# Kernel tuning notes

Hardware: AMD Instinct MI355X
Metric: run time of the kernel (lower is better)

Reference implementation:

```python
import jax, jax.numpy as jnp
import numpy as np


def conv1x1(x, w, b):
    # x: (B,C,H,W), w: (O,C), b: (O,) -- 1x1 conv == channel matmul
    return jnp.einsum('bchw,oc->bohw', x, w) + b[None, :, None, None]


def setup_inputs() -> dict:
    key = jax.random.key(0)
    B, C, H, W = 4, 256, 64, 64
    Ch = C // 2
    ks = jax.random.split(key, 12)
    s = 0.05
    return {
        'x':    jax.random.normal(ks[0], (B, C, H, W), jnp.float32),
        'wf1':  jax.random.normal(ks[1], (Ch, C), jnp.float32) * s,
        'bf1':  jnp.zeros((Ch,), jnp.float32),
        'wf2':  jax.random.normal(ks[2], (Ch, Ch), jnp.float32) * s,
        'bf2':  jnp.zeros((Ch,), jnp.float32),
        'wg1':  jax.random.normal(ks[3], (Ch, C), jnp.float32) * s,
        'bg1':  jnp.zeros((Ch,), jnp.float32),
        'wg2':  jax.random.normal(ks[4], (Ch, Ch), jnp.float32) * s,
        'bg2':  jnp.zeros((Ch,), jnp.float32),
        'wh':   jax.random.normal(ks[5], (C, C), jnp.float32) * s,
        'bh':   jnp.zeros((C,), jnp.float32),
        'gamma': jnp.full((1,), 0.5, jnp.float32),
    }


def reference(x, wf1, bf1, wf2, bf2, wg1, bg1, wg2, bg2, wh, bh, gamma):
    B, C, H, W = x.shape
    N = H * W
    # f_ and g_: conv1x1 -> relu -> conv1x1, projecting C -> C/2
    f = conv1x1(jax.nn.relu(conv1x1(x, wf1, bf1)), wf2, bf2).reshape(B, -1, N)  # (B,C/2,N)
    g = conv1x1(jax.nn.relu(conv1x1(x, wg1, bg1)), wg2, bg2).reshape(B, -1, N)  # (B,C/2,N)
    h = conv1x1(x, wh, bh).reshape(B, C, N)                                     # (B,C,N)
    # attn_dist = bmm(f^T, g): (B, N, N)
    attn = jnp.einsum('bcn,bcm->bnm', f, g)
    # softmax over dim=1 (the query axis) -- non-standard axis, as in source
    attn_soft = jax.nn.softmax(attn, axis=1)
    out = jnp.einsum('bcn,bnm->bcm', h, attn_soft).reshape(B, C, H, W)
    out = gamma[0] * out + x  # skip connection
    return out, attn_soft.reshape(B, H, W, N)
```

## Files before the change

### kernel.cpp

```cpp
#include <hip/hip_runtime.h>

typedef unsigned short u16;
typedef unsigned int   u32;
typedef float  floatx4 __attribute__((ext_vector_type(4)));
typedef __bf16 bfx8    __attribute__((ext_vector_type(8)));
typedef u16    u16x8   __attribute__((ext_vector_type(8)));

#define DEV __device__ __forceinline__

#define NB 4
#define NC 256
#define NCH 128
#define NSP 4096
#define OUT_OFF 4194304

DEV u16 f2bf(float f) {
  u32 u = __builtin_bit_cast(u32, f);
  u = (u + 0x7fffu + ((u >> 16) & 1u)) >> 16;
  return (u16)u;
}

DEV float bf2f(u16 h) {
  u32 w = (u32)h << 16;
  return __builtin_bit_cast(float, w);
}

DEV void lds_load16(const u16* g, u16* l) {
  __builtin_amdgcn_global_load_lds(
      (const __attribute__((address_space(1))) u32*)g,
      (__attribute__((address_space(3))) u32*)l, 16, 0, 0);
}

DEV floatx4 mfma16(bfx8 a, bfx8 b, floatx4 c) {
  return __builtin_amdgcn_mfma_f32_16x16x32_bf16(a, b, c, 0, 0, 0);
}

DEV float rsum16(float v) {
  #pragma unroll
  for (int m = 1; m < 16; m <<= 1) v += __shfl_xor(v, m, 64);
  return v;
}

__global__ __launch_bounds__(256) void cvt_all(
    const float* __restrict__ wf1, const float* __restrict__ wg1,
    const float* __restrict__ wf2, const float* __restrict__ wg2,
    const float* __restrict__ wh,
    u16* __restrict__ wfg1b, u16* __restrict__ wfg2b, u16* __restrict__ whb,
    float* __restrict__ rs,
    const float* __restrict__ bf1, const float* __restrict__ bg1,
    const float* __restrict__ bf2, const float* __restrict__ bg2,
    float* __restrict__ bfg1, float* __restrict__ bfg2) {
  int i = blockIdx.x * 256 + threadIdx.x;
  if (i < 32768) { wfg1b[i] = f2bf(wf1[i]); return; }
  i -= 32768;
  if (i < 32768) { wfg1b[32768 + i] = f2bf(wg1[i]); return; }
  i -= 32768;
  if (i < 16384) { wfg2b[i] = f2bf(wf2[i]); return; }
  i -= 16384;
  if (i < 16384) { wfg2b[16384 + i] = f2bf(wg2[i]); return; }
  i -= 16384;
  if (i < 65536) { whb[i] = f2bf(wh[i]); return; }
  i -= 65536;
  if (i < NB * NSP) { rs[i] = 0.f; return; }
  i -= NB * NSP;
  if (i < 128) { bfg1[i] = bf1[i]; return; }
  i -= 128;
  if (i < 128) { bfg1[128 + i] = bg1[i]; return; }
  i -= 128;
  if (i < 128) { bfg2[i] = bf2[i]; return; }
  i -= 128;
  if (i < 128) { bfg2[128 + i] = bg2[i]; return; }
}

__global__ __launch_bounds__(256) void transpose_x(const float* __restrict__ x,
                                                   u16* __restrict__ xT) {
  __shared__ float T[64 * 65];
  const int b = blockIdx.z, c0 = blockIdx.y * 64, n0 = blockIdx.x * 64;
  const int tid = threadIdx.x;
  const int j = tid & 63, r0 = tid >> 6;
  const size_t xbase = ((size_t)b * NC + c0) * NSP + n0;
  #pragma unroll
  for (int s = 0; s < 16; s++) {
    int cl = s * 4 + r0;
    T[cl * 65 + j] = x[xbase + (size_t)cl * NSP + j];
  }
  __syncthreads();
  const size_t tbase = ((size_t)b * NSP + n0) * NC + c0;
  #pragma unroll
  for (int s = 0; s < 16; s++) {
    int nr = s * 4 + r0;
    xT[tbase + (size_t)nr * NC + j] = f2bf(T[j * 65 + nr]);
  }
}

template<int BM, int BN, int BK, int BIAS, bool RELU, bool OUTBF16, bool FINAL,
         bool SWZ>
__global__ __launch_bounds__(256) void gemm_bt_k(
    const u16* __restrict__ A, long long sA, int lda,
    const u16* __restrict__ Bt, long long sB, int ldb,
    void* __restrict__ C, long long sC, int ldc,
    int K, const float* __restrict__ bias, int sbias,
    const float* __restrict__ gamma, const float* __restrict__ xres,
    const float* __restrict__ rsv) {
  constexpr int TM = BM / 32, TN = BN / 32, KS = BK / 32;
  constexpr int ASZ = BM * BK, BSZ = BN * BK;
  __shared__ u16 As[2][ASZ];
  __shared__ u16 Bs[2][BSZ];
  int bx = blockIdx.x, by = blockIdx.y, bz = blockIdx.z;
  if constexpr (SWZ) {
    const int gx = gridDim.x, gy = gridDim.y;
    const int nwg = gx * gy * gridDim.z;
    const int bid = (bz * gy + by) * gx + bx;
    const int lx = (bid & 7) * (nwg >> 3) + (bid >> 3);
    bx = lx % gx;
    const int t = lx / gx;
    by = t % gy;
    bz = t / gy;
  }
  const int b = bz;
  const u16* Ab = A + (size_t)sA * b;
  const u16* Bb = Bt + (size_t)sB * b;
  const int m0 = bx * BM, n0 = by * BN;
  const int tid = threadIdx.x, lane = tid & 63, wave = tid >> 6;
  const int q = lane >> 4, cc = lane & 15;
  const int wm = (wave >> 1) * (BM / 2), wn = (wave & 1) * (BN / 2);

  auto stage = [&](int p, int k0) {
    #pragma unroll
    for (int i = 0; i < ASZ / 2048; i++) {
      int slot = i * 256 + tid;
      int fr = slot / (64 * KS);
      int ks = (slot / 64) % KS;
      int qq = (slot >> 4) & 3, cq = slot & 15;
      lds_load16(Ab + (size_t)(m0 + fr * 16 + cq) * lda + k0 + ks * 32 + qq * 8,
                 &As[p][slot * 8]);
    }
    #pragma unroll
    for (int i = 0; i < BSZ / 2048; i++) {
      int slot = i * 256 + tid;
      int fr = slot / (64 * KS);
      int ks = (slot / 64) % KS;
      int qq = (slot >> 4) & 3, cq = slot & 15;
      lds_load16(Bb + (size_t)(n0 + fr * 16 + cq) * ldb + k0 + ks * 32 + qq * 8,
                 &Bs[p][slot * 8]);
    }
  };

  floatx4 acc[TM][TN];
  #pragma unroll
  for (int mi = 0; mi < TM; mi++)
    #pragma unroll
    for (int ni = 0; ni < TN; ni++)
      acc[mi][ni] = floatx4{0.f, 0.f, 0.f, 0.f};

  stage(0, 0);
  __syncthreads();
  int p = 0;
  for (int k0 = 0; k0 < K; k0 += BK) {
    if (k0 + BK < K) stage(p ^ 1, k0 + BK);
    #pragma unroll
    for (int ks = 0; ks < KS; ks++) {
      bfx8 af[TM], bfr[TN];
      #pragma unroll
      for (int mi = 0; mi < TM; mi++)
        af[mi] = *(const bfx8*)(&As[p][((((wm >> 4) + mi) * KS + ks) * 64 + lane) * 8]);
      #pragma unroll
      for (int ni = 0; ni < TN; ni++)
        bfr[ni] = *(const bfx8*)(&Bs[p][((((wn >> 4) + ni) * KS + ks) * 64 + lane) * 8]);
      #pragma unroll
      for (int mi = 0; mi < TM; mi++)
        #pragma unroll
        for (int ni = 0; ni < TN; ni++)
          acc[mi][ni] = mfma16(af[mi], bfr[ni], acc[mi][ni]);
    }
    __syncthreads();
    p ^= 1;
  }

  float g0 = 0.f;
  if constexpr (FINAL) g0 = gamma[0];
  #pragma unroll
  for (int mi = 0; mi < TM; mi++) {
    #pragma unroll
    for (int ni = 0; ni < TN; ni++) {
      const int col = n0 + wn + ni * 16 + cc;
      float scl = 0.f;
      if constexpr (FINAL) scl = g0 / rsv[(size_t)b * NSP + col];
      #pragma unroll
      for (int r = 0; r < 4; r++) {
        int row = m0 + wm + mi * 16 + q * 4 + r;
        float v = acc[mi][ni][r];
        if constexpr (BIAS == 1) v += bias[b * sbias + col];
        if constexpr (BIAS == 2) v += bias[b * sbias + row];
        if constexpr (RELU) v = fmaxf(v, 0.f);
        size_t idx = (size_t)sC * b + (size_t)row * ldc + col;
        if constexpr (FINAL) v = v * scl + xres[idx];
        if constexpr (OUTBF16) ((u16*)C)[idx] = f2bf(v);
        else ((float*)C)[idx] = v;
      }
    }
  }
}

__global__ __launch_bounds__(256) void attn_se_k(
    const u16* __restrict__ gT, const u16* __restrict__ fT,
    float* __restrict__ rsum, u16* __restrict__ pT) {
  __shared__ u16 Bs[64 * 128];
  __shared__ u16 Pb[64 * 72];
  const int b = blockIdx.z, m0 = blockIdx.y * 64, n0 = blockIdx.x * 512;
  const int tid = threadIdx.x, lane = tid & 63, wave = tid >> 6;
  const int q = lane >> 4, cc = lane & 15;
  const size_t bN = (size_t)b * NSP;

  bfx8 af[4];
  {
    const u16* gA = gT + (bN + m0 + wave * 16 + cc) * NCH;
    #pragma unroll
    for (int ks = 0; ks < 4; ks++) af[ks] = *(const bfx8*)(gA + ks * 32 + q * 8);
  }
  float ps[4] = {0.f, 0.f, 0.f, 0.f};

  for (int sc = 0; sc < 8; sc++) {
    const int nc = n0 + sc * 64;
    #pragma unroll
    for (int i = 0; i < 4; i++) {
      int slot = i * 256 + tid;
      int ni = slot >> 8, ks = (slot >> 6) & 3;
      int qq = (slot >> 4) & 3, cq = slot & 15;
      lds_load16(fT + (bN + nc + ni * 16 + cq) * NCH + ks * 32 + qq * 8,
                 Bs + slot * 8);
    }
    __syncthreads();
    #pragma unroll
    for (int ni = 0; ni < 4; ni++) {
      floatx4 s = floatx4{0.f, 0.f, 0.f, 0.f};
      #pragma unroll
      for (int ks = 0; ks < 4; ks++) {
        bfx8 bfr = *(const bfx8*)(Bs + ((ni * 4 + ks) * 64 + lane) * 8);
        s = mfma16(af[ks], bfr, s);
      }
      #pragma unroll
      for (int r = 0; r < 4; r++) {
        float e = __expf(fminf(s[r], 80.f));
        ps[r] += e;
        Pb[(wave * 16 + q * 4 + r) * 72 + ni * 16 + cc] = f2bf(e);
      }
    }
    __syncthreads();
    #pragma unroll
    for (int i = 0; i < 2; i++) {
      int slot = i * 256 + tid;
      int ml = slot >> 3, c8 = slot & 7;
      u16x8 v = *(const u16x8*)(Pb + ml * 72 + c8 * 8);
      *(u16x8*)(pT + (bN + m0 + ml) * NSP + nc + c8 * 8) = v;
    }
  }
  #pragma unroll
  for (int r = 0; r < 4; r++) ps[r] = rsum16(ps[r]);
  if (cc == 0) {
    #pragma unroll
    for (int r = 0; r < 4; r++)
      atomicAdd(&rsum[bN + m0 + wave * 16 + q * 4 + r], ps[r]);
  }
}

__global__ __launch_bounds__(256) void attn_norm_k(
    const u16* __restrict__ pT, const float* __restrict__ rs,
    float* __restrict__ outP) {
  __shared__ u16 T[64 * 257];
  __shared__ float rinvs[256];
  const int b = blockIdx.z, n0 = blockIdx.x * 64, m0 = blockIdx.y * 256;
  const int tid = threadIdx.x;
  const size_t bN = (size_t)b * NSP;

  rinvs[tid] = 1.f / rs[bN + m0 + tid];
  #pragma unroll
  for (int i = 0; i < 8; i++) {
    int slot = i * 256 + tid;
    int mi = slot >> 3, c8 = slot & 7;
    u16x8 v = *(const u16x8*)(pT + (bN + m0 + mi) * NSP + n0 + c8 * 8);
    #pragma unroll
    for (int j = 0; j < 8; j++) T[(c8 * 8 + j) * 257 + mi] = v[j];
  }
  __syncthreads();
  #pragma unroll
  for (int i = 0; i < 16; i++) {
    int slot = i * 256 + tid;
    int nl = slot >> 6, f4 = slot & 63;
    floatx4 rv = *(const floatx4*)(rinvs + f4 * 4);
    const u16* tr = T + nl * 257 + f4 * 4;
    floatx4 o;
    #pragma unroll
    for (int k = 0; k < 4; k++) o[k] = bf2f(tr[k]) * rv[k];
    *(floatx4*)(outP + (bN + n0 + nl) * NSP + m0 + f4 * 4) = o;
  }
}

extern "C" void kernel_launch(void* const* d_in, const int* in_sizes, int n_in,
                              void* d_out, int out_size, void* d_ws, size_t ws_size,
                              hipStream_t stream) {
  const float* x     = (const float*)d_in[0];
  const float* wf1   = (const float*)d_in[1];
  const float* bf1   = (const float*)d_in[2];
  const float* wf2   = (const float*)d_in[3];
  const float* bf2   = (const float*)d_in[4];
  const float* wg1   = (const float*)d_in[5];
  const float* bg1   = (const float*)d_in[6];
  const float* wg2   = (const float*)d_in[7];
  const float* bg2   = (const float*)d_in[8];
  const float* wh    = (const float*)d_in[9];
  const float* bh    = (const float*)d_in[10];
  const float* gamma = (const float*)d_in[11];
  float* out = (float*)d_out;

  char* ws = (char*)d_ws;
  size_t off = 0;
  auto alloc = [&](size_t bytes) -> char* {
    char* p = ws + off;
    off += (bytes + 255) & ~(size_t)255;
    return p;
  };
  u16* wfg1b = (u16*)alloc((size_t)256 * 256 * 2);
  u16* wfg2b = (u16*)alloc((size_t)2 * 128 * 128 * 2);
  u16* whb   = (u16*)alloc((size_t)NC * NC * 2);
  float* bfg1 = (float*)alloc(256 * 4);
  float* bfg2 = (float*)alloc(256 * 4);
  u16* xT   = (u16*)alloc((size_t)NB * NSP * NC * 2);
  u16* fg1T = (u16*)alloc((size_t)NB * NSP * 256 * 2);
  u16* fTb  = (u16*)alloc((size_t)NB * NSP * NCH * 2);
  u16* gTb  = (u16*)alloc((size_t)NB * NSP * NCH * 2);
  u16* hb   = (u16*)alloc((size_t)NB * NC * NSP * 2);
  float* rs = (float*)alloc((size_t)NB * NSP * 4);
  u16* pTb  = (u16*)alloc((size_t)NB * NSP * NSP * 2);

  cvt_all<<<dim3(707), 256, 0, stream>>>(wf1, wg1, wf2, wg2, wh,
                                         wfg1b, wfg2b, whb,
                                         rs, bf1, bg1, bf2, bg2, bfg1, bfg2);
  transpose_x<<<dim3(NSP / 64, NC / 64, NB), 256, 0, stream>>>(x, xT);

  const long long sX = (long long)NSP * NC;
  const long long sH = (long long)NC * NSP;
  const long long sP = (long long)NSP * NSP;
  const long long sFG = (long long)NB * NSP * NCH;

  gemm_bt_k<64, 128, 64, 1, true, true, false, false>
      <<<dim3(256, 2, 1), 256, 0, stream>>>(
      xT, 0, NC, wfg1b, 0, NC, fg1T, 0, 256, NC, bfg1, 0,
      nullptr, nullptr, nullptr);
  gemm_bt_k<64, 128, 64, 1, false, true, false, false>
      <<<dim3(256, 1, 2), 256, 0, stream>>>(
      fg1T, 128, 256, wfg2b, 128 * 128, NCH, fTb, sFG, NCH, NCH, bfg2, 128,
      nullptr, nullptr, nullptr);
  gemm_bt_k<64, 128, 64, 2, false, true, false, false>
      <<<dim3(4, 32, NB), 256, 0, stream>>>(
      whb, 0, NC, xT, sX, NC, hb, sH, NSP, NC, bh, 0,
      nullptr, nullptr, nullptr);

  attn_se_k<<<dim3(8, 64, NB), 256, 0, stream>>>(gTb, fTb, rs, pTb);

  gemm_bt_k<128, 64, 64, 0, false, false, true, true>
      <<<dim3(2, 64, NB), 256, 0, stream>>>(
      hb, sH, NSP, pTb, sP, NSP, out, sH, NSP, NSP, nullptr, 0,
      gamma, x, rs);

  attn_norm_k<<<dim3(NSP / 64, NSP / 256, NB), 256, 0, stream>>>(
      pTb, rs, out + OUT_OFF);

  (void)in_sizes; (void)n_in; (void)out_size; (void)ws_size;
}
```

Measured before the change: 494.9 us.

## Fuse score/exp kernel with output GEMM into single attention kernel

Replaces the separate exp-score kernel (with atomic row sums) and the final h·P GEMM with one kernel. For each 64-column query block it computes the scores over all key tiles, exponentiates them, and immediately multiplies them by h tiles staged in LDS. The softmax denominators are accumulated locally, which removes the atomics and the zeroing pass. This avoids re-reading the full bf16 P matrix in the output GEMM, but P is still written for the normalized attention output. In exchange, each block now serializes 64 tiles with two barriers per tile and has only 256 blocks of 512 threads, so occupancy may be lower.

```diff
diff --git a/kernel.cpp b/kernel.cpp
--- a/kernel.cpp
+++ b/kernel.cpp
@@ -5,6 +5,7 @@
 typedef float  floatx4 __attribute__((ext_vector_type(4)));
 typedef __bf16 bfx8    __attribute__((ext_vector_type(8)));
 typedef u16    u16x8   __attribute__((ext_vector_type(8)));
+typedef u32    u32x4   __attribute__((ext_vector_type(4)));
 
 #define DEV __device__ __forceinline__
 
@@ -35,18 +36,11 @@
   return __builtin_amdgcn_mfma_f32_16x16x32_bf16(a, b, c, 0, 0, 0);
 }
 
-DEV float rsum16(float v) {
-  #pragma unroll
-  for (int m = 1; m < 16; m <<= 1) v += __shfl_xor(v, m, 64);
-  return v;
-}
-
 __global__ __launch_bounds__(256) void cvt_all(
     const float* __restrict__ wf1, const float* __restrict__ wg1,
     const float* __restrict__ wf2, const float* __restrict__ wg2,
     const float* __restrict__ wh,
     u16* __restrict__ wfg1b, u16* __restrict__ wfg2b, u16* __restrict__ whb,
-    float* __restrict__ rs,
     const float* __restrict__ bf1, const float* __restrict__ bg1,
     const float* __restrict__ bf2, const float* __restrict__ bg2,
     float* __restrict__ bfg1, float* __restrict__ bfg2) {
@@ -61,8 +55,6 @@
   i -= 16384;
   if (i < 65536) { whb[i] = f2bf(wh[i]); return; }
   i -= 65536;
-  if (i < NB * NSP) { rs[i] = 0.f; return; }
-  i -= NB * NSP;
   if (i < 128) { bfg1[i] = bf1[i]; return; }
   i -= 128;
   if (i < 128) { bfg1[128 + i] = bg1[i]; return; }
@@ -93,34 +85,20 @@
   }
 }
 
-template<int BM, int BN, int BK, int BIAS, bool RELU, bool OUTBF16, bool FINAL,
-         bool SWZ>
+template<int BM, int BN, int BK, int BIAS, bool RELU, bool OUTBF16>
 __global__ __launch_bounds__(256) void gemm_bt_k(
     const u16* __restrict__ A, long long sA, int lda,
     const u16* __restrict__ Bt, long long sB, int ldb,
     void* __restrict__ C, long long sC, int ldc,
-    int K, const float* __restrict__ bias, int sbias,
-    const float* __restrict__ gamma, const float* __restrict__ xres,
-    const float* __restrict__ rsv) {
+    int K, const float* __restrict__ bias, int sbias) {
   constexpr int TM = BM / 32, TN = BN / 32, KS = BK / 32;
   constexpr int ASZ = BM * BK, BSZ = BN * BK;
   __shared__ u16 As[2][ASZ];
   __shared__ u16 Bs[2][BSZ];
-  int bx = blockIdx.x, by = blockIdx.y, bz = blockIdx.z;
-  if constexpr (SWZ) {
-    const int gx = gridDim.x, gy = gridDim.y;
-    const int nwg = gx * gy * gridDim.z;
-    const int bid = (bz * gy + by) * gx + bx;
-    const int lx = (bid & 7) * (nwg >> 3) + (bid >> 3);
-    bx = lx % gx;
-    const int t = lx / gx;
-    by = t % gy;
-    bz = t / gy;
-  }
-  const int b = bz;
+  const int b = blockIdx.z;
   const u16* Ab = A + (size_t)sA * b;
   const u16* Bb = Bt + (size_t)sB * b;
-  const int m0 = bx * BM, n0 = by * BN;
+  const int m0 = blockIdx.x * BM, n0 = blockIdx.y * BN;
   const int tid = threadIdx.x, lane = tid & 63, wave = tid >> 6;
   const int q = lane >> 4, cc = lane & 15;
   const int wm = (wave >> 1) * (BM / 2), wn = (wave & 1) * (BN / 2);
@@ -177,15 +155,11 @@
     p ^= 1;
   }
 
-  float g0 = 0.f;
-  if constexpr (FINAL) g0 = gamma[0];
   #pragma unroll
   for (int mi = 0; mi < TM; mi++) {
     #pragma unroll
     for (int ni = 0; ni < TN; ni++) {
       const int col = n0 + wn + ni * 16 + cc;
-      float scl = 0.f;
-      if constexpr (FINAL) scl = g0 / rsv[(size_t)b * NSP + col];
       #pragma unroll
       for (int r = 0; r < 4; r++) {
         int row = m0 + wm + mi * 16 + q * 4 + r;
@@ -194,7 +168,6 @@
         if constexpr (BIAS == 2) v += bias[b * sbias + row];
         if constexpr (RELU) v = fmaxf(v, 0.f);
         size_t idx = (size_t)sC * b + (size_t)row * ldc + col;
-        if constexpr (FINAL) v = v * scl + xres[idx];
         if constexpr (OUTBF16) ((u16*)C)[idx] = f2bf(v);
         else ((float*)C)[idx] = v;
       }
@@ -202,65 +175,143 @@
   }
 }
 
-__global__ __launch_bounds__(256) void attn_se_k(
+__global__ __launch_bounds__(512) void attn_out_k(
     const u16* __restrict__ gT, const u16* __restrict__ fT,
-    float* __restrict__ rsum, u16* __restrict__ pT) {
-  __shared__ u16 Bs[64 * 128];
-  __shared__ u16 Pb[64 * 72];
-  const int b = blockIdx.z, m0 = blockIdx.y * 64, n0 = blockIdx.x * 512;
-  const int tid = threadIdx.x, lane = tid & 63, wave = tid >> 6;
+    const u16* __restrict__ hb, float* __restrict__ rs,
+    u16* __restrict__ pT, float* __restrict__ out,
+    const float* __restrict__ gamma, const float* __restrict__ x) {
+  __shared__ u16 fTl[2][64 * 128];
+  __shared__ u16 hl[256 * 64];
+  __shared__ u32 EL[2048];
+  __shared__ float rsp[8][16];
+  __shared__ float rsinv[64];
+  const int b = blockIdx.z, m0 = blockIdx.x * 64;
+  const int tid = threadIdx.x, lane = tid & 63, w = tid >> 6;
   const int q = lane >> 4, cc = lane & 15;
+  const int khalf = w >> 2, m16w = w & 3;
   const size_t bN = (size_t)b * NSP;
 
-  bfx8 af[4];
+  bfx8 gB[4];
   {
-    const u16* gA = gT + (bN + m0 + wave * 16 + cc) * NCH;
-    #pragma unroll
-    for (int ks = 0; ks < 4; ks++) af[ks] = *(const bfx8*)(gA + ks * 32 + q * 8);
-  }
-  float ps[4] = {0.f, 0.f, 0.f, 0.f};
-
-  for (int sc = 0; sc < 8; sc++) {
-    const int nc = n0 + sc * 64;
+    const u16* gA = gT + (bN + m0 + m16w * 16 + cc) * NCH;
+    #pragma unroll
+    for (int ks = 0; ks < 4; ks++) gB[ks] = *(const bfx8*)(gA + ks * 32 + q * 8);
+  }
+
+  floatx4 oacc[2][4];
+  #pragma unroll
+  for (int cg = 0; cg < 2; cg++)
+    #pragma unroll
+    for (int m16 = 0; m16 < 4; m16++)
+      oacc[cg][m16] = floatx4{0.f, 0.f, 0.f, 0.f};
+  float ps = 0.f;
+
+  auto stage_f = [&](int buf, int nt) {
+    #pragma unroll
+    for (int i = 0; i < 2; i++) {
+      int slot = i * 512 + tid;
+      int fr = slot >> 8, ks = (slot >> 6) & 3;
+      int qq = (slot >> 4) & 3, cq = slot & 15;
+      lds_load16(fT + (bN + nt + fr * 16 + cq) * NCH + ks * 32 + qq * 8,
+                 &fTl[buf][slot * 8]);
+    }
+  };
+  auto stage_h = [&](int nt) {
     #pragma unroll
     for (int i = 0; i < 4; i++) {
-      int slot = i * 256 + tid;
-      int ni = slot >> 8, ks = (slot >> 6) & 3;
+      int slot = i * 512 + tid;
+      int fr = slot >> 7, ks = (slot >> 6) & 1;
       int qq = (slot >> 4) & 3, cq = slot & 15;
-      lds_load16(fT + (bN + nc + ni * 16 + cq) * NCH + ks * 32 + qq * 8,
-                 Bs + slot * 8);
+      lds_load16(hb + ((size_t)b * NC + fr * 16 + cq) * NSP + nt + ks * 32 + qq * 8,
+                 &hl[slot * 8]);
+    }
+  };
+
+  stage_f(0, 0);
+  __syncthreads();
+
+  #pragma unroll 1
+  for (int t = 0; t < 64; t++) {
+    const int nt = t * 64;
+    if (t + 1 < 64) stage_f((t + 1) & 1, nt + 64);
+    stage_h(nt);
+
+    floatx4 sacc[2];
+    sacc[0] = floatx4{0.f, 0.f, 0.f, 0.f};
+    sacc[1] = floatx4{0.f, 0.f, 0.f, 0.f};
+    #pragma unroll
+    for (int ks = 0; ks < 4; ks++) {
+      #pragma unroll
+      for (int ni = 0; ni < 2; ni++) {
+        bfx8 a = *(const bfx8*)(&fTl[t & 1][(((khalf * 2 + ni) * 4 + ks) * 64 + lane) * 8]);
+        sacc[ni] = mfma16(a, gB[ks], sacc[ni]);
+      }
+    }
+    #pragma unroll
+    for (int ni = 0; ni < 2; ni++) {
+      float e[4];
+      #pragma unroll
+      for (int r = 0; r < 4; r++) {
+        e[r] = __expf(fminf(sacc[ni][r], 80.f));
+        ps += e[r];
+      }
+      #pragma unroll
+      for (int r2 = 0; r2 < 2; r2++) {
+        u32 pk = (u32)f2bf(e[2 * r2]) | ((u32)f2bf(e[2 * r2 + 1]) << 16);
+        EL[((m16w * 2 + khalf) * 64 + (2 * ni + (q >> 1)) * 16 + cc) * 4 +
+           2 * (q & 1) + r2] = pk;
+      }
     }
     __syncthreads();
-    #pragma unroll
-    for (int ni = 0; ni < 4; ni++) {
-      floatx4 s = floatx4{0.f, 0.f, 0.f, 0.f};
-      #pragma unroll
-      for (int ks = 0; ks < 4; ks++) {
-        bfx8 bfr = *(const bfx8*)(Bs + ((ni * 4 + ks) * 64 + lane) * 8);
-        s = mfma16(af[ks], bfr, s);
-      }
+
+    #pragma unroll
+    for (int ks = 0; ks < 2; ks++) {
+      bfx8 bf[4];
+      #pragma unroll
+      for (int m16 = 0; m16 < 4; m16++)
+        bf[m16] = *(const bfx8*)((const u16*)&EL[((m16 * 2 + ks) * 64 + lane) * 4]);
+      #pragma unroll
+      for (int cg = 0; cg < 2; cg++) {
+        bfx8 a = *(const bfx8*)(&hl[(((w * 2 + cg) * 2 + ks) * 64 + lane) * 8]);
+        #pragma unroll
+        for (int m16 = 0; m16 < 4; m16++)
+          oacc[cg][m16] = mfma16(a, bf[m16], oacc[cg][m16]);
+      }
+    }
+    {
+      const int fr = tid >> 7, ks2 = (tid >> 6) & 1;
+      const int qv = (tid >> 4) & 3, cv = tid & 15;
+      u32x4 d = *(const u32x4*)(&EL[tid * 4]);
+      *(u32x4*)(pT + (bN + m0 + fr * 16 + cv) * NSP + nt + ks2 * 32 + qv * 8) = d;
+    }
+    __syncthreads();
+  }
+
+  ps += __shfl_xor(ps, 16, 64);
+  ps += __shfl_xor(ps, 32, 64);
+  if (lane < 16) rsp[w][lane] = ps;
+  __syncthreads();
+  if (tid < 64) {
+    float s = rsp[tid >> 4][tid & 15] + rsp[4 + (tid >> 4)][tid & 15];
+    rs[bN + m0 + tid] = s;
+    rsinv[tid] = 1.f / s;
+  }
+  __syncthreads();
+
+  const float g0 = gamma[0];
+  #pragma unroll
+  for (int cg = 0; cg < 2; cg++) {
+    #pragma unroll
+    for (int m16 = 0; m16 < 4; m16++) {
+      const float ri = rsinv[m16 * 16 + cc];
       #pragma unroll
       for (int r = 0; r < 4; r++) {
-        float e = __expf(fminf(s[r], 80.f));
-        ps[r] += e;
-        Pb[(wave * 16 + q * 4 + r) * 72 + ni * 16 + cc] = f2bf(e);
-      }
-    }
-    __syncthreads();
-    #pragma unroll
-    for (int i = 0; i < 2; i++) {
-      int slot = i * 256 + tid;
-      int ml = slot >> 3, c8 = slot & 7;
-      u16x8 v = *(const u16x8*)(Pb + ml * 72 + c8 * 8);
-      *(u16x8*)(pT + (bN + m0 + ml) * NSP + nc + c8 * 8) = v;
-    }
-  }
-  #pragma unroll
-  for (int r = 0; r < 4; r++) ps[r] = rsum16(ps[r]);
-  if (cc == 0) {
-    #pragma unroll
-    for (int r = 0; r < 4; r++)
-      atomicAdd(&rsum[bN + m0 + wave * 16 + q * 4 + r], ps[r]);
+        int c = w * 32 + cg * 16 + q * 4 + r;
+        int m = m16 * 16 + cc;
+        size_t idx = ((size_t)b * NC + c) * NSP + m0 + m;
+        out[idx] = g0 * oacc[cg][m16][r] * ri + x[idx];
+      }
+    }
   }
 }
 
@@ -333,35 +384,24 @@
   float* rs = (float*)alloc((size_t)NB * NSP * 4);
   u16* pTb  = (u16*)alloc((size_t)NB * NSP * NSP * 2);
 
-  cvt_all<<<dim3(707), 256, 0, stream>>>(wf1, wg1, wf2, wg2, wh,
+  cvt_all<<<dim3(641), 256, 0, stream>>>(wf1, wg1, wf2, wg2, wh,
                                          wfg1b, wfg2b, whb,
-                                         rs, bf1, bg1, bf2, bg2, bfg1, bfg2);
+                                         bf1, bg1, bf2, bg2, bfg1, bfg2);
   transpose_x<<<dim3(NSP / 64, NC / 64, NB), 256, 0, stream>>>(x, xT);
 
   const long long sX = (long long)NSP * NC;
   const long long sH = (long long)NC * NSP;
-  const long long sP = (long long)NSP * NSP;
   const long long sFG = (long long)NB * NSP * NCH;
 
-  gemm_bt_k<64, 128, 64, 1, true, true, false, false>
-      <<<dim3(256, 2, 1), 256, 0, stream>>>(
-      xT, 0, NC, wfg1b, 0, NC, fg1T, 0, 256, NC, bfg1, 0,
-      nullptr, nullptr, nullptr);
-  gemm_bt_k<64, 128, 64, 1, false, true, false, false>
-      <<<dim3(256, 1, 2), 256, 0, stream>>>(
-      fg1T, 128, 256, wfg2b, 128 * 128, NCH, fTb, sFG, NCH, NCH, bfg2, 128,
-      nullptr, nullptr, nullptr);
-  gemm_bt_k<64, 128, 64, 2, false, true, false, false>
-      <<<dim3(4, 32, NB), 256, 0, stream>>>(
-      whb, 0, NC, xT, sX, NC, hb, sH, NSP, NC, bh, 0,
-      nullptr, nullptr, nullptr);
-
-  attn_se_k<<<dim3(8, 64, NB), 256, 0, stream>>>(gTb, fTb, rs, pTb);
-
-  gemm_bt_k<128, 64, 64, 0, false, false, true, true>
-      <<<dim3(2, 64, NB), 256, 0, stream>>>(
-      hb, sH, NSP, pTb, sP, NSP, out, sH, NSP, NSP, nullptr, 0,
-      gamma, x, rs);
+  gemm_bt_k<64, 128, 64, 1, true, true><<<dim3(256, 2, 1), 256, 0, stream>>>(
+      xT, 0, NC, wfg1b, 0, NC, fg1T, 0, 256, NC, bfg1, 0);
+  gemm_bt_k<64, 128, 64, 1, false, true><<<dim3(256, 1, 2), 256, 0, stream>>>(
+      fg1T, 128, 256, wfg2b, 128 * 128, NCH, fTb, sFG, NCH, NCH, bfg2, 128);
+  gemm_bt_k<64, 128, 64, 2, false, true><<<dim3(4, 32, NB), 256, 0, stream>>>(
+      whb, 0, NC, xT, sX, NC, hb, sH, NSP, NC, bh, 0);
+
+  attn_out_k<<<dim3(NSP / 64, 1, NB), 512, 0, stream>>>(
+      gTb, fTb, hb, rs, pTb, out, gamma, x);
 
   attn_norm_k<<<dim3(NSP / 64, NSP / 256, NB), 256, 0, stream>>>(
       pTb, rs, out + OUT_OFF);
```

After: 533.1 us. +7.7%, slower.

## Split-K the final attention GEMM, add reduce kernel, drop LDS double buffering

Applied to the files above, without the earlier changes.

The final h·P GEMM (K=4096, 512 blocks) is split into two K halves, each writing fp32 partials, and a new reduce kernel sums them and applies the gamma/rowsum scaling and residual. This doubles the block count to fill more CUs, at the cost of extra partial-buffer traffic and one more kernel launch. The GEMM also drops its double-buffered LDS staging for a single buffer with a sync before compute, which lowers LDS use but exposes load latency. f2bf now uses the compiler's native bf16 conversion.

```diff
diff --git a/kernel.cpp b/kernel.cpp
--- a/kernel.cpp
+++ b/kernel.cpp
@@ -13,11 +13,10 @@
 #define NCH 128
 #define NSP 4096
 #define OUT_OFF 4194304
+#define KSPL 2
 
 DEV u16 f2bf(float f) {
-  u32 u = __builtin_bit_cast(u32, f);
-  u = (u + 0x7fffu + ((u >> 16) & 1u)) >> 16;
-  return (u16)u;
+  return __builtin_bit_cast(u16, (__bf16)f);
 }
 
 DEV float bf2f(u16 h) {
@@ -93,19 +92,16 @@
   }
 }
 
-template<int BM, int BN, int BK, int BIAS, bool RELU, bool OUTBF16, bool FINAL,
+template<int BM, int BN, int BK, int BIAS, bool RELU, bool OUTBF16, int KSP,
          bool SWZ>
 __global__ __launch_bounds__(256) void gemm_bt_k(
     const u16* __restrict__ A, long long sA, int lda,
     const u16* __restrict__ Bt, long long sB, int ldb,
     void* __restrict__ C, long long sC, int ldc,
-    int K, const float* __restrict__ bias, int sbias,
-    const float* __restrict__ gamma, const float* __restrict__ xres,
-    const float* __restrict__ rsv) {
+    int K, const float* __restrict__ bias, int sbias) {
   constexpr int TM = BM / 32, TN = BN / 32, KS = BK / 32;
-  constexpr int ASZ = BM * BK, BSZ = BN * BK;
-  __shared__ u16 As[2][ASZ];
-  __shared__ u16 Bs[2][BSZ];
+  __shared__ u16 As[BM * BK];
+  __shared__ u16 Bs[BN * BK];
   int bx = blockIdx.x, by = blockIdx.y, bz = blockIdx.z;
   if constexpr (SWZ) {
     const int gx = gridDim.x, gy = gridDim.y;
@@ -117,56 +113,51 @@
     by = t % gy;
     bz = t / gy;
   }
-  const int b = bz;
-  const u16* Ab = A + (size_t)sA * b;
-  const u16* Bb = Bt + (size_t)sB * b;
+  const int b = (KSP > 1) ? bz / KSP : bz;
+  const int kc = (KSP > 1) ? bz % KSP : 0;
+  const u16* Ab = A + (size_t)sA * b + (size_t)kc * K;
+  const u16* Bb = Bt + (size_t)sB * b + (size_t)kc * K;
   const int m0 = bx * BM, n0 = by * BN;
   const int tid = threadIdx.x, lane = tid & 63, wave = tid >> 6;
   const int q = lane >> 4, cc = lane & 15;
   const int wm = (wave >> 1) * (BM / 2), wn = (wave & 1) * (BN / 2);
 
-  auto stage = [&](int p, int k0) {
-    #pragma unroll
-    for (int i = 0; i < ASZ / 2048; i++) {
+  floatx4 acc[TM][TN];
+  #pragma unroll
+  for (int mi = 0; mi < TM; mi++)
+    #pragma unroll
+    for (int ni = 0; ni < TN; ni++)
+      acc[mi][ni] = floatx4{0.f, 0.f, 0.f, 0.f};
+
+  for (int k0 = 0; k0 < K; k0 += BK) {
+    #pragma unroll
+    for (int i = 0; i < BM * BK / 2048; i++) {
       int slot = i * 256 + tid;
       int fr = slot / (64 * KS);
       int ks = (slot / 64) % KS;
       int qq = (slot >> 4) & 3, cq = slot & 15;
       lds_load16(Ab + (size_t)(m0 + fr * 16 + cq) * lda + k0 + ks * 32 + qq * 8,
-                 &As[p][slot * 8]);
-    }
-    #pragma unroll
-    for (int i = 0; i < BSZ / 2048; i++) {
+                 As + slot * 8);
+    }
+    #pragma unroll
+    for (int i = 0; i < BN * BK / 2048; i++) {
       int slot = i * 256 + tid;
       int fr = slot / (64 * KS);
       int ks = (slot / 64) % KS;
       int qq = (slot >> 4) & 3, cq = slot & 15;
       lds_load16(Bb + (size_t)(n0 + fr * 16 + cq) * ldb + k0 + ks * 32 + qq * 8,
-                 &Bs[p][slot * 8]);
-    }
-  };
-
-  floatx4 acc[TM][TN];
-  #pragma unroll
-  for (int mi = 0; mi < TM; mi++)
-    #pragma unroll
-    for (int ni = 0; ni < TN; ni++)
-      acc[mi][ni] = floatx4{0.f, 0.f, 0.f, 0.f};
-
-  stage(0, 0);
-  __syncthreads();
-  int p = 0;
-  for (int k0 = 0; k0 < K; k0 += BK) {
-    if (k0 + BK < K) stage(p ^ 1, k0 + BK);
+                 Bs + slot * 8);
+    }
+    __syncthreads();
     #pragma unroll
     for (int ks = 0; ks < KS; ks++) {
       bfx8 af[TM], bfr[TN];
       #pragma unroll
       for (int mi = 0; mi < TM; mi++)
-        af[mi] = *(const bfx8*)(&As[p][((((wm >> 4) + mi) * KS + ks) * 64 + lane) * 8]);
+        af[mi] = *(const bfx8*)(As + ((((wm >> 4) + mi) * KS + ks) * 64 + lane) * 8);
       #pragma unroll
       for (int ni = 0; ni < TN; ni++)
-        bfr[ni] = *(const bfx8*)(&Bs[p][((((wn >> 4) + ni) * KS + ks) * 64 + lane) * 8]);
+        bfr[ni] = *(const bfx8*)(Bs + ((((wn >> 4) + ni) * KS + ks) * 64 + lane) * 8);
       #pragma unroll
       for (int mi = 0; mi < TM; mi++)
         #pragma unroll
@@ -174,18 +165,13 @@
           acc[mi][ni] = mfma16(af[mi], bfr[ni], acc[mi][ni]);
     }
     __syncthreads();
-    p ^= 1;
-  }
-
-  float g0 = 0.f;
-  if constexpr (FINAL) g0 = gamma[0];
+  }
+
   #pragma unroll
   for (int mi = 0; mi < TM; mi++) {
     #pragma unroll
     for (int ni = 0; ni < TN; ni++) {
       const int col = n0 + wn + ni * 16 + cc;
-      float scl = 0.f;
-      if constexpr (FINAL) scl = g0 / rsv[(size_t)b * NSP + col];
       #pragma unroll
       for (int r = 0; r < 4; r++) {
         int row = m0 + wm + mi * 16 + q * 4 + r;
@@ -193,8 +179,7 @@
         if constexpr (BIAS == 1) v += bias[b * sbias + col];
         if constexpr (BIAS == 2) v += bias[b * sbias + row];
         if constexpr (RELU) v = fmaxf(v, 0.f);
-        size_t idx = (size_t)sC * b + (size_t)row * ldc + col;
-        if constexpr (FINAL) v = v * scl + xres[idx];
+        size_t idx = (size_t)sC * bz + (size_t)row * ldc + col;
         if constexpr (OUTBF16) ((u16*)C)[idx] = f2bf(v);
         else ((float*)C)[idx] = v;
       }
@@ -262,6 +247,26 @@
     for (int r = 0; r < 4; r++)
       atomicAdd(&rsum[bN + m0 + wave * 16 + q * 4 + r], ps[r]);
   }
+}
+
+__global__ __launch_bounds__(256) void reduce_out_k(
+    const float* __restrict__ part, const float* __restrict__ rs,
+    const float* __restrict__ x, const float* __restrict__ gamma,
+    float* __restrict__ out) {
+  const float g0 = gamma[0];
+  const size_t idx = ((size_t)blockIdx.x * 256 + threadIdx.x) * 4;
+  const int m = (int)(idx & (NSP - 1));
+  const int b = (int)(idx >> 20);
+  const size_t inner = idx & (((size_t)1 << 20) - 1);
+  const size_t SC = (size_t)NC * NSP;
+  floatx4 p0 = *(const floatx4*)(part + (size_t)(b * KSPL) * SC + inner);
+  floatx4 p1 = *(const floatx4*)(part + (size_t)(b * KSPL + 1) * SC + inner);
+  floatx4 xr = *(const floatx4*)(x + idx);
+  floatx4 rv = *(const floatx4*)(rs + (size_t)b * NSP + m);
+  floatx4 o;
+  #pragma unroll
+  for (int k = 0; k < 4; k++) o[k] = g0 * (p0[k] + p1[k]) / rv[k] + xr[k];
+  *(floatx4*)(out + idx) = o;
 }
 
 __global__ __launch_bounds__(256) void attn_norm_k(
@@ -332,6 +337,7 @@
   u16* hb   = (u16*)alloc((size_t)NB * NC * NSP * 2);
   float* rs = (float*)alloc((size_t)NB * NSP * 4);
   u16* pTb  = (u16*)alloc((size_t)NB * NSP * NSP * 2);
+  float* part = (float*)alloc((size_t)NB * KSPL * NC * NSP * 4);
 
   cvt_all<<<dim3(707), 256, 0, stream>>>(wf1, wg1, wf2, wg2, wh,
                                          wfg1b, wfg2b, whb,
@@ -343,25 +349,23 @@
   const long long sP = (long long)NSP * NSP;
   const long long sFG = (long long)NB * NSP * NCH;
 
-  gemm_bt_k<64, 128, 64, 1, true, true, false, false>
+  gemm_bt_k<64, 128, 64, 1, true, true, 1, false>
       <<<dim3(256, 2, 1), 256, 0, stream>>>(
-      xT, 0, NC, wfg1b, 0, NC, fg1T, 0, 256, NC, bfg1, 0,
-      nullptr, nullptr, nullptr);
-  gemm_bt_k<64, 128, 64, 1, false, true, false, false>
+      xT, 0, NC, wfg1b, 0, NC, fg1T, 0, 256, NC, bfg1, 0);
+  gemm_bt_k<64, 128, 64, 1, false, true, 1, false>
       <<<dim3(256, 1, 2), 256, 0, stream>>>(
-      fg1T, 128, 256, wfg2b, 128 * 128, NCH, fTb, sFG, NCH, NCH, bfg2, 128,
-      nullptr, nullptr, nullptr);
-  gemm_bt_k<64, 128, 64, 2, false, true, false, false>
+      fg1T, 128, 256, wfg2b, 128 * 128, NCH, fTb, sFG, NCH, NCH, bfg2, 128);
+  gemm_bt_k<64, 128, 64, 2, false, true, 1, false>
       <<<dim3(4, 32, NB), 256, 0, stream>>>(
-      whb, 0, NC, xT, sX, NC, hb, sH, NSP, NC, bh, 0,
-      nullptr, nullptr, nullptr);
+      whb, 0, NC, xT, sX, NC, hb, sH, NSP, NC, bh, 0);
 
   attn_se_k<<<dim3(8, 64, NB), 256, 0, stream>>>(gTb, fTb, rs, pTb);
 
-  gemm_bt_k<128, 64, 64, 0, false, false, true, true>
-      <<<dim3(2, 64, NB), 256, 0, stream>>>(
-      hb, sH, NSP, pTb, sP, NSP, out, sH, NSP, NSP, nullptr, 0,
-      gamma, x, rs);
+  gemm_bt_k<128, 64, 64, 0, false, false, KSPL, true>
+      <<<dim3(2, 64, NB * KSPL), 256, 0, stream>>>(
+      hb, sH, NSP, pTb, sP, NSP, part, sH, NSP, NSP / KSPL, nullptr, 0);
+
+  reduce_out_k<<<dim3(4096), 256, 0, stream>>>(part, rs, x, gamma, out);
 
   attn_norm_k<<<dim3(NSP / 64, NSP / 256, NB), 256, 0, stream>>>(
       pTb, rs, out + OUT_OFF);
```

Measured after the change: 512.6 us. 3.6% more time.
